# Kernel optimization log

Hardware: AMD Instinct MI355X
Metric: run time of the kernel (lower is better)

Reference implementation:

```python
import jax, jax.numpy as jnp
import numpy as np

LL = 1 << 20            # Fastfood padded size (power of 2 >= DD)
DD = 1024 * 768         # out_features * in_features
OUT, IN = 1024, 768


def fwht(v):
    """Unnormalized fast Walsh-Hadamard transform over a length-2^k vector."""
    n = v.shape[0]
    h = 1
    while h < n:
        v = v.reshape(-1, 2, h)
        v = jnp.concatenate([v[:, 0] + v[:, 1], v[:, 0] - v[:, 1]], axis=-1)
        h *= 2
    return v.reshape(n)


def setup_inputs() -> dict:
    key = jax.random.key(0)
    ks = jax.random.split(key, 7)
    x = jax.random.normal(ks[0], (8, 2048, IN), dtype=jnp.float32)
    theta = jax.random.normal(ks[1], (2048,), dtype=jnp.float32)
    W_0 = jax.random.normal(ks[2], (OUT, IN), dtype=jnp.float32) * 0.02
    b = jax.random.normal(ks[3], (OUT,), dtype=jnp.float32) * 0.02
    # Rademacher +/-1 diagonal
    BB = (jax.random.bernoulli(ks[4], 0.5, (LL,)).astype(jnp.float32) * 2.0 - 1.0)
    GG = jax.random.normal(ks[5], (LL,), dtype=jnp.float32)
    Pi = jax.random.permutation(ks[6], LL).astype(jnp.int64)
    return {"x": x, "theta": theta, "W_0": W_0, "b": b, "BB": BB, "GG": GG, "Pi": Pi}


def reference(x, theta, W_0, b, BB, GG, Pi):
    # pad intrinsic parameter to LL (theta.numel() < LL branch)
    theta_pad = jnp.zeros((LL,), dtype=theta.dtype).at[: theta.shape[0]].set(theta)
    # Fastfood: H B theta -> permute -> G diag -> H
    v = fwht(BB * theta_pad)
    v = v[Pi] * GG
    v = fwht(v)
    divisor = jnp.sqrt(LL * jnp.sum(GG * GG))
    update_vec = v[:DD] / (divisor * np.sqrt(float(DD) / LL))
    W_eff = W_0 + update_vec.reshape(OUT, IN)
    return jnp.einsum("bsi,oi->bso", x, W_eff) + b
```

## Files before the change

kernel.cpp:

```cpp
#include <hip/hip_runtime.h>
#include <hip/hip_bf16.h>


#define LL (1 << 20)
#define DD (1024 * 768)
#define OUTF 1024
#define INF 768
#define MROWS 16384

typedef __attribute__((ext_vector_type(8))) short s16x8;
typedef __attribute__((ext_vector_type(4))) float f32x4;
typedef __attribute__((ext_vector_type(16))) float f32x16;

__device__ __forceinline__ unsigned short f2bf(float f) {
    union { float f; unsigned u; } v; v.f = f;
    unsigned r = v.u + 0x7FFF + ((v.u >> 16) & 1);
    return (unsigned short)(r >> 16);
}

__device__ __forceinline__ unsigned cvt_pk_bf16(float lo, float hi) {
    unsigned r;
    asm("v_cvt_pk_bf16_f32 %0, %1, %2" : "=v"(r) : "v"(lo), "v"(hi));
    return r;
}

__global__ __launch_bounds__(1024)
void k3_gather_fwht_lo(const int* __restrict__ Pi, const float* __restrict__ GG,
                       const float* __restrict__ BB, const float* __restrict__ theta,
                       f32x4* __restrict__ T2, float* __restrict__ partial) {
    __shared__ float r01s[2048];
    __shared__ f32x4 sA[1024];
    __shared__ float sB[4 * 1028];
    __shared__ float ws[16];
    const int t = threadIdx.x;
    const int s_r = t >> 8, tt = t & 255, lane = t & 63;
    const int row = blockIdx.x * 4 + s_r;

    const int4   pv = ((const int4*)Pi)[row * 256 + tt];
    const float4 gv = ((const float4*)GG)[row * 256 + tt];

    float w0 = BB[t] * theta[t];
    float w1 = BB[t + 1024] * theta[t + 1024];
    #pragma unroll
    for (int j = 0; j < 6; j++) {
        const float sgn = ((lane >> j) & 1) ? -1.0f : 1.0f;
        float o0 = __shfl_xor(w0, 1 << j, 64);
        float o1 = __shfl_xor(w1, 1 << j, 64);
        w0 = fmaf(sgn, w0, o0);
        w1 = fmaf(sgn, w1, o1);
    }
    float2* sr = (float2*)sB;
    sr[t] = make_float2(w0, w1);
    __syncthreads();
    {
        const int b = t & ~192;
        const float2 q00 = sr[b], q10 = sr[b + 64], q01 = sr[b + 128], q11 = sr[b + 192];
        const float s6 = (t & 64) ? -1.0f : 1.0f;
        const float s7 = (t & 128) ? -1.0f : 1.0f;
        w0 = (q00.x + s7 * q01.x) + s6 * (q10.x + s7 * q11.x);
        w1 = (q00.y + s7 * q01.y) + s6 * (q10.y + s7 * q11.y);
    }
    __syncthreads();
    sr[t] = make_float2(w0, w1);
    float g2 = gv.x * gv.x + gv.y * gv.y + gv.z * gv.z + gv.w * gv.w;
    #pragma unroll
    for (int o = 32; o > 0; o >>= 1) g2 += __shfl_down(g2, o, 64);
    if (lane == 0) ws[t >> 6] = g2;
    __syncthreads();
    {
        const int b = t & ~768;
        const float2 q00 = sr[b], q10 = sr[b + 256], q01 = sr[b + 512], q11 = sr[b + 768];
        const float s8 = (t & 256) ? -1.0f : 1.0f;
        const float s9 = (t & 512) ? -1.0f : 1.0f;
        w0 = (q00.x + s9 * q01.x) + s8 * (q10.x + s9 * q11.x);
        w1 = (q00.y + s9 * q01.y) + s8 * (q10.y + s9 * q11.y);
    }
    r01s[t] = w0;
    r01s[1024 + t] = w1;
    __syncthreads();

    float v[4];
    {
        int p; float g;
        p = pv.x; g = gv.x;
        v[0] = (r01s[p & 1023] + (((p >> 10) & 1) ? -1.0f : 1.0f) * r01s[1024 + (p & 1023)]) * g;
        p = pv.y; g = gv.y;
        v[1] = (r01s[p & 1023] + (((p >> 10) & 1) ? -1.0f : 1.0f) * r01s[1024 + (p & 1023)]) * g;
        p = pv.z; g = gv.z;
        v[2] = (r01s[p & 1023] + (((p >> 10) & 1) ? -1.0f : 1.0f) * r01s[1024 + (p & 1023)]) * g;
        p = pv.w; g = gv.w;
        v[3] = (r01s[p & 1023] + (((p >> 10) & 1) ? -1.0f : 1.0f) * r01s[1024 + (p & 1023)]) * g;
    }
    float a;
    a = v[0]; v[0] = a + v[1]; v[1] = a - v[1];
    a = v[2]; v[2] = a + v[3]; v[3] = a - v[3];
    a = v[0]; v[0] = a + v[2]; v[2] = a - v[2];
    a = v[1]; v[1] = a + v[3]; v[3] = a - v[3];
    #pragma unroll
    for (int j = 0; j < 6; j++) {
        const float sgn = ((lane >> j) & 1) ? -1.0f : 1.0f;
        #pragma unroll
        for (int c = 0; c < 4; c++) {
            float o = __shfl_xor(v[c], 1 << j, 64);
            v[c] = fmaf(sgn, v[c], o);
        }
    }
    {
        f32x4 vv; vv.x = v[0]; vv.y = v[1]; vv.z = v[2]; vv.w = v[3];
        sA[t] = vv;
    }
    __syncthreads();
    {
        const int b = t & ~192;
        const f32x4 q00 = sA[b];
        const f32x4 q10 = sA[b + 64];
        const f32x4 q01 = sA[b + 128];
        const f32x4 q11 = sA[b + 192];
        const float s8 = (tt & 64) ? -1.0f : 1.0f;
        const float s9 = (tt & 128) ? -1.0f : 1.0f;
        #pragma unroll
        for (int c = 0; c < 4; c++)
            v[c] = (q00[c] + s9 * q01[c]) + s8 * (q10[c] + s9 * q11[c]);
    }
    if (t == 0) {
        float s = 0;
        #pragma unroll
        for (int i = 0; i < 16; i++) s += ws[i];
        partial[blockIdx.x] = s;
    }
    {
        f32x4 vv; vv.x = v[0]; vv.y = v[1]; vv.z = v[2]; vv.w = v[3];
        *(f32x4*)&sB[s_r * 1028 + 4 * tt] = vv;
    }
    __syncthreads();
    {
        const int rl = t & 3;
        const int lo4 = t >> 2;
        const f32x4 w = *(const f32x4*)&sB[rl * 1028 + lo4 * 4];
        T2[(size_t)lo4 * 1024 + blockIdx.x * 4 + rl] = w;
    }
}

__global__ __launch_bounds__(1024)
void k4_fwht_hi(const f32x4* __restrict__ T2, const float* __restrict__ partial,
                const float* __restrict__ W0, ushort* __restrict__ WB) {
    __shared__ f32x4 sx[1024];
    __shared__ float rw[17];
    const int t = threadIdx.x;
    const int g = blockIdx.x;
    const int lane = t & 63;

    float pr = 0.0f;
    if (t < 256) pr = partial[t];
    #pragma unroll
    for (int o = 32; o > 0; o >>= 1) pr += __shfl_down(pr, o, 64);
    if (t < 256 && lane == 0) rw[t >> 6] = pr;

    f32x4 vv = T2[(size_t)g * 1024 + t];
    #pragma unroll
    for (int j = 0; j < 6; j++) {
        const float sgn = ((lane >> j) & 1) ? -1.0f : 1.0f;
        #pragma unroll
        for (int c = 0; c < 4; c++) {
            float o = __shfl_xor(vv[c], 1 << j, 64);
            vv[c] = fmaf(sgn, vv[c], o);
        }
    }
    sx[t] = vv;
    __syncthreads();
    if (t == 0) rw[16] = rw[0] + rw[1] + rw[2] + rw[3];
    {
        const int b = t & ~192;
        const f32x4 q00 = sx[b];
        const f32x4 q10 = sx[b + 64];
        const f32x4 q01 = sx[b + 128];
        const f32x4 q11 = sx[b + 192];
        const float s6 = (t & 64) ? -1.0f : 1.0f;
        const float s7 = (t & 128) ? -1.0f : 1.0f;
        #pragma unroll
        for (int c = 0; c < 4; c++)
            vv[c] = (q00[c] + s7 * q01[c]) + s6 * (q10[c] + s7 * q11[c]);
    }
    __syncthreads();
    sx[t] = vv;
    __syncthreads();
    {
        const int b = t & ~768;
        const f32x4 q00 = sx[b];
        const f32x4 q10 = sx[b + 256];
        const f32x4 q01 = sx[b + 512];
        const f32x4 q11 = sx[b + 768];
        const float s8 = (t & 256) ? -1.0f : 1.0f;
        const float s9 = (t & 512) ? -1.0f : 1.0f;
        #pragma unroll
        for (int c = 0; c < 4; c++)
            vv[c] = (q00[c] + s9 * q01[c]) + s8 * (q10[c] + s9 * q11[c]);
    }
    if (t < 768) {
        const float scale = rsqrtf(rw[16] * (float)DD);
        const size_t d = (size_t)t * 1024 + 4 * g;
        const float4 w = *(const float4*)&W0[d];
        ushort4 o;
        o.x = f2bf(w.x + vv.x * scale);
        o.y = f2bf(w.y + vv.y * scale);
        o.z = f2bf(w.z + vv.z * scale);
        o.w = f2bf(w.w + vv.w * scale);
        *(ushort4*)&WB[d] = o;
    }
}

#define BM 128
#define BN 128
#define BK 64
#define KITERS (INF / BK)

__global__ __launch_bounds__(256)
void k7_gemm(const float* __restrict__ A, const ushort* __restrict__ B,
             const float* __restrict__ bias, float* __restrict__ C) {
    __shared__ ushort As[2][BM * BK];
    __shared__ ushort Bs[2][BN * BK];
    const int tid  = threadIdx.x;
    const int lane = tid & 63;
    const int wave = tid >> 6;
    const int n0 = blockIdx.x * BN;
    const int m0 = blockIdx.y * BM;
    const int wm = (wave & 1) * 64;
    const int wn = (wave >> 1) * 64;

    const int fr_row = lane & 31;
    const int fr_kh  = lane >> 5;

    f32x16 acc[2][2];
    #pragma unroll
    for (int i = 0; i < 2; i++)
        #pragma unroll
        for (int j = 0; j < 2; j++) acc[i][j] = (f32x16)(0.0f);

    int arow[4], akc[4];
    #pragma unroll
    for (int j = 0; j < 4; j++) {
        const int s = j * 256 + tid;
        arow[j] = s >> 3;
        akc[j]  = (s & 7) ^ (arow[j] & 7);
    }

    f32x4 ar[8];
    auto loadA = [&](int kt) {
        #pragma unroll
        for (int j = 0; j < 4; j++) {
            const float* ga = A + (size_t)(m0 + arow[j]) * INF + kt + akc[j] * 8;
            ar[2 * j]     = *(const f32x4*)ga;
            ar[2 * j + 1] = *(const f32x4*)(ga + 4);
        }
    };
    auto writeA = [&](int bsel) {
        #pragma unroll
        for (int j = 0; j < 4; j++) {
            union { s16x8 v; unsigned u[4]; } o;
            const f32x4 lo = ar[2 * j], hi = ar[2 * j + 1];
            o.u[0] = cvt_pk_bf16(lo.x, lo.y);
            o.u[1] = cvt_pk_bf16(lo.z, lo.w);
            o.u[2] = cvt_pk_bf16(hi.x, hi.y);
            o.u[3] = cvt_pk_bf16(hi.z, hi.w);
            *(s16x8*)&As[bsel][(j * 256 + tid) * 8] = o.v;
        }
    };
    auto stageB = [&](int bsel, int kt) {
        #pragma unroll
        for (int i = 0; i < 4; i++) {
            const int s   = i * 256 + tid;
            const int row = s >> 3;
            const int kc  = (s & 7) ^ (row & 7);
            const ushort* gb = B + (size_t)(n0 + row) * INF + kt + kc * 8;
            __builtin_amdgcn_global_load_lds(
                (const __attribute__((address_space(1))) void*)gb,
                (__attribute__((address_space(3))) void*)&Bs[bsel][i * 2048 + wave * 512], 16, 0, 0);
        }
    };

    loadA(0);
    stageB(0, 0);
    writeA(0);
    __syncthreads();

    for (int t = 0; t < KITERS; t++) {
        const int cur = t & 1;
        const bool pf = (t + 1 < KITERS);
        if (pf) {
            loadA((t + 1) * BK);
            stageB(cur ^ 1, (t + 1) * BK);
        }

        const ushort* Ab = As[cur];
        const ushort* Bb = Bs[cur];
        #pragma unroll
        for (int ks = 0; ks < 4; ks++) {
            const int kc = ks * 2 + fr_kh;
            s16x8 af[2], bf[2];
            #pragma unroll
            for (int mi = 0; mi < 2; mi++) {
                const int r = wm + mi * 32 + fr_row;
                af[mi] = *(const s16x8*)&Ab[(r * 8 + (kc ^ (r & 7))) * 8];
            }
            #pragma unroll
            for (int ni = 0; ni < 2; ni++) {
                const int r = wn + ni * 32 + fr_row;
                bf[ni] = *(const s16x8*)&Bb[(r * 8 + (kc ^ (r & 7))) * 8];
            }
            #pragma unroll
            for (int mi = 0; mi < 2; mi++)
                #pragma unroll
                for (int ni = 0; ni < 2; ni++)
                    acc[mi][ni] = __builtin_amdgcn_mfma_f32_32x32x16_bf16(
                        af[mi], bf[ni], acc[mi][ni], 0, 0, 0);
        }
        if (pf) writeA(cur ^ 1);
        __syncthreads();
    }

    const int ccol = lane & 31;
    const int rbase = (lane >> 5) * 4;
    #pragma unroll
    for (int ni = 0; ni < 2; ni++) {
        const int n = n0 + wn + ni * 32 + ccol;
        const float bv = bias[n];
        #pragma unroll
        for (int mi = 0; mi < 2; mi++) {
            const int mb = m0 + wm + mi * 32 + rbase;
            #pragma unroll
            for (int r = 0; r < 16; r++) {
                const int m = mb + (r & 3) + 8 * (r >> 2);
                C[(size_t)m * OUTF + n] = acc[mi][ni][r] + bv;
            }
        }
    }
}

extern "C" void kernel_launch(void* const* d_in, const int* in_sizes, int n_in,
                              void* d_out, int out_size, void* d_ws, size_t ws_size,
                              hipStream_t stream) {
    (void)in_sizes; (void)n_in; (void)out_size; (void)ws_size;
    const float* x     = (const float*)d_in[0];
    const float* theta = (const float*)d_in[1];
    const float* W0    = (const float*)d_in[2];
    const float* bias  = (const float*)d_in[3];
    const float* BB    = (const float*)d_in[4];
    const float* GG    = (const float*)d_in[5];
    const int*   Pi    = (const int*)d_in[6];
    float* out = (float*)d_out;

    char* ws = (char*)d_ws;
    f32x4*  T2   = (f32x4*)ws;
    ushort* WB   = (ushort*)(ws + 4194304);
    float*  PART = (float*)(ws + 5767168);

    k3_gather_fwht_lo<<<256, 1024, 0, stream>>>(Pi, GG, BB, theta, T2, PART);
    k4_fwht_hi      <<<256, 1024, 0, stream>>>(T2, PART, W0, WB);
    k7_gemm<<<dim3(OUTF/BN, MROWS/BM), 256, 0, stream>>>(x, WB, bias, out);
}
```

Measured before the change: 185.8 us.

## Pre-convert activations to bf16 inside FWHT kernels and use direct LDS loads in GEMM

Moves the fp32-to-bf16 conversion of x out of the GEMM and into the two Fastfood FWHT kernels, each converting half of x into a bf16 workspace buffer. The GEMM then stages both A and B with global_load_lds at BK=32, dropping the register round-trip and in-loop conversion for A. It also swaps the grid so blocks walk M first. The cost is an extra write and read of a 25 MB bf16 copy of x, and the smaller K tile means more barriers per block.

```diff
diff --git a/kernel.cpp b/kernel.cpp
--- a/kernel.cpp
+++ b/kernel.cpp
@@ -27,6 +27,7 @@
 __global__ __launch_bounds__(1024)
 void k3_gather_fwht_lo(const int* __restrict__ Pi, const float* __restrict__ GG,
                        const float* __restrict__ BB, const float* __restrict__ theta,
+                       const float* __restrict__ X, ushort* __restrict__ XB,
                        f32x4* __restrict__ T2, float* __restrict__ partial) {
     __shared__ float r01s[2048];
     __shared__ f32x4 sA[1024];
@@ -139,11 +140,29 @@
         const f32x4 w = *(const f32x4*)&sB[rl * 1028 + lo4 * 4];
         T2[(size_t)lo4 * 1024 + blockIdx.x * 4 + rl] = w;
     }
+
+    {
+        const f32x4* X4 = (const f32x4*)X;
+        s16x8* O = (s16x8*)XB;
+        size_t u = (size_t)blockIdx.x * 3072 + t;
+        #pragma unroll
+        for (int j = 0; j < 3; j++, u += 1024) {
+            const f32x4 A4 = X4[2 * u];
+            const f32x4 B4 = X4[2 * u + 1];
+            union { s16x8 v; unsigned w4[4]; } o;
+            o.w4[0] = cvt_pk_bf16(A4.x, A4.y);
+            o.w4[1] = cvt_pk_bf16(A4.z, A4.w);
+            o.w4[2] = cvt_pk_bf16(B4.x, B4.y);
+            o.w4[3] = cvt_pk_bf16(B4.z, B4.w);
+            O[u] = o.v;
+        }
+    }
 }
 
 __global__ __launch_bounds__(1024)
 void k4_fwht_hi(const f32x4* __restrict__ T2, const float* __restrict__ partial,
-                const float* __restrict__ W0, ushort* __restrict__ WB) {
+                const float* __restrict__ W0, ushort* __restrict__ WB,
+                const float* __restrict__ X, ushort* __restrict__ XB) {
     __shared__ f32x4 sx[1024];
     __shared__ float rw[17];
     const int t = threadIdx.x;
@@ -207,23 +226,40 @@
         o.w = f2bf(w.w + vv.w * scale);
         *(ushort4*)&WB[d] = o;
     }
+
+    {
+        const f32x4* X4 = (const f32x4*)X;
+        s16x8* O = (s16x8*)XB;
+        size_t u = 786432 + (size_t)g * 3072 + t;
+        #pragma unroll
+        for (int j = 0; j < 3; j++, u += 1024) {
+            const f32x4 A4 = X4[2 * u];
+            const f32x4 B4 = X4[2 * u + 1];
+            union { s16x8 v; unsigned w4[4]; } o;
+            o.w4[0] = cvt_pk_bf16(A4.x, A4.y);
+            o.w4[1] = cvt_pk_bf16(A4.z, A4.w);
+            o.w4[2] = cvt_pk_bf16(B4.x, B4.y);
+            o.w4[3] = cvt_pk_bf16(B4.z, B4.w);
+            O[u] = o.v;
+        }
+    }
 }
 
 #define BM 128
 #define BN 128
-#define BK 64
+#define BK 32
 #define KITERS (INF / BK)
 
 __global__ __launch_bounds__(256)
-void k7_gemm(const float* __restrict__ A, const ushort* __restrict__ B,
+void k7_gemm(const ushort* __restrict__ A, const ushort* __restrict__ B,
              const float* __restrict__ bias, float* __restrict__ C) {
     __shared__ ushort As[2][BM * BK];
     __shared__ ushort Bs[2][BN * BK];
     const int tid  = threadIdx.x;
     const int lane = tid & 63;
     const int wave = tid >> 6;
-    const int n0 = blockIdx.x * BN;
-    const int m0 = blockIdx.y * BM;
+    const int m0 = blockIdx.x * BM;
+    const int n0 = blockIdx.y * BN;
     const int wm = (wave & 1) * 64;
     const int wn = (wave >> 1) * 64;
 
@@ -236,76 +272,45 @@
         #pragma unroll
         for (int j = 0; j < 2; j++) acc[i][j] = (f32x16)(0.0f);
 
-    int arow[4], akc[4];
-    #pragma unroll
-    for (int j = 0; j < 4; j++) {
-        const int s = j * 256 + tid;
-        arow[j] = s >> 3;
-        akc[j]  = (s & 7) ^ (arow[j] & 7);
-    }
-
-    f32x4 ar[8];
-    auto loadA = [&](int kt) {
-        #pragma unroll
-        for (int j = 0; j < 4; j++) {
-            const float* ga = A + (size_t)(m0 + arow[j]) * INF + kt + akc[j] * 8;
-            ar[2 * j]     = *(const f32x4*)ga;
-            ar[2 * j + 1] = *(const f32x4*)(ga + 4);
-        }
-    };
-    auto writeA = [&](int bsel) {
-        #pragma unroll
-        for (int j = 0; j < 4; j++) {
-            union { s16x8 v; unsigned u[4]; } o;
-            const f32x4 lo = ar[2 * j], hi = ar[2 * j + 1];
-            o.u[0] = cvt_pk_bf16(lo.x, lo.y);
-            o.u[1] = cvt_pk_bf16(lo.z, lo.w);
-            o.u[2] = cvt_pk_bf16(hi.x, hi.y);
-            o.u[3] = cvt_pk_bf16(hi.z, hi.w);
-            *(s16x8*)&As[bsel][(j * 256 + tid) * 8] = o.v;
-        }
-    };
-    auto stageB = [&](int bsel, int kt) {
-        #pragma unroll
-        for (int i = 0; i < 4; i++) {
+    auto stage = [&](int bsel, int kt) {
+        #pragma unroll
+        for (int i = 0; i < 2; i++) {
             const int s   = i * 256 + tid;
-            const int row = s >> 3;
-            const int kc  = (s & 7) ^ (row & 7);
+            const int row = s >> 2;
+            const int kc  = (s & 3) ^ (row & 3);
+            const ushort* ga = A + (size_t)(m0 + row) * INF + kt + kc * 8;
             const ushort* gb = B + (size_t)(n0 + row) * INF + kt + kc * 8;
+            __builtin_amdgcn_global_load_lds(
+                (const __attribute__((address_space(1))) void*)ga,
+                (__attribute__((address_space(3))) void*)&As[bsel][i * 2048 + wave * 512], 16, 0, 0);
             __builtin_amdgcn_global_load_lds(
                 (const __attribute__((address_space(1))) void*)gb,
                 (__attribute__((address_space(3))) void*)&Bs[bsel][i * 2048 + wave * 512], 16, 0, 0);
         }
     };
 
-    loadA(0);
-    stageB(0, 0);
-    writeA(0);
+    stage(0, 0);
     __syncthreads();
 
     for (int t = 0; t < KITERS; t++) {
         const int cur = t & 1;
-        const bool pf = (t + 1 < KITERS);
-        if (pf) {
-            loadA((t + 1) * BK);
-            stageB(cur ^ 1, (t + 1) * BK);
-        }
+        if (t + 1 < KITERS) stage(cur ^ 1, (t + 1) * BK);
 
         const ushort* Ab = As[cur];
         const ushort* Bb = Bs[cur];
         #pragma unroll
-        for (int ks = 0; ks < 4; ks++) {
+        for (int ks = 0; ks < 2; ks++) {
             const int kc = ks * 2 + fr_kh;
             s16x8 af[2], bf[2];
             #pragma unroll
             for (int mi = 0; mi < 2; mi++) {
                 const int r = wm + mi * 32 + fr_row;
-                af[mi] = *(const s16x8*)&Ab[(r * 8 + (kc ^ (r & 7))) * 8];
+                af[mi] = *(const s16x8*)&Ab[(r * 4 + (kc ^ (r & 3))) * 8];
             }
             #pragma unroll
             for (int ni = 0; ni < 2; ni++) {
                 const int r = wn + ni * 32 + fr_row;
-                bf[ni] = *(const s16x8*)&Bb[(r * 8 + (kc ^ (r & 7))) * 8];
+                bf[ni] = *(const s16x8*)&Bb[(r * 4 + (kc ^ (r & 3))) * 8];
             }
             #pragma unroll
             for (int mi = 0; mi < 2; mi++)
@@ -314,7 +319,6 @@
                     acc[mi][ni] = __builtin_amdgcn_mfma_f32_32x32x16_bf16(
                         af[mi], bf[ni], acc[mi][ni], 0, 0, 0);
         }
-        if (pf) writeA(cur ^ 1);
         __syncthreads();
     }
 
@@ -350,11 +354,12 @@
     float* out = (float*)d_out;
 
     char* ws = (char*)d_ws;
-    f32x4*  T2   = (f32x4*)ws;
-    ushort* WB   = (ushort*)(ws + 4194304);
-    float*  PART = (float*)(ws + 5767168);
-
-    k3_gather_fwht_lo<<<256, 1024, 0, stream>>>(Pi, GG, BB, theta, T2, PART);
-    k4_fwht_hi      <<<256, 1024, 0, stream>>>(T2, PART, W0, WB);
-    k7_gemm<<<dim3(OUTF/BN, MROWS/BM), 256, 0, stream>>>(x, WB, bias, out);
-}
+    ushort* XB   = (ushort*)ws;
+    f32x4*  T2   = (f32x4*)(ws + 25165824);
+    ushort* WB   = (ushort*)(ws + 29360128);
+    float*  PART = (float*)(ws + 30932992);
+
+    k3_gather_fwht_lo<<<256, 1024, 0, stream>>>(Pi, GG, BB, theta, x, XB, T2, PART);
+    k4_fwht_hi      <<<256, 1024, 0, stream>>>(T2, PART, W0, WB, x, XB);
+    k7_gemm<<<dim3(MROWS/BM, OUTF/BN), 256, 0, stream>>>(XB, WB, bias, out);
+}
```

New measurement: 178.2 us. 1.04x faster.
